# Kernel optimization log

Measured on AMD Instinct MI355X. Metric: run time of the kernel, lower is better.

The kernel has to match this reference:

```python
import jax, jax.numpy as jnp
import numpy as np

D_MODEL, D_STATE, EXPAND, D_CONV, HEADDIM = 1024, 128, 2, 4, 64
D_INNER = EXPAND * D_MODEL                      # 2048
NHEADS = D_INNER // HEADDIM                     # 32
NGROUPS = 1
CONV_DIM = D_INNER + 2 * NGROUPS * D_STATE      # 2304
D_IN_PROJ = 2 * D_INNER + 2 * NGROUPS * D_STATE + NHEADS  # 4384
BATCH, SEQ = 2, 4096
EPS = 1e-5


def setup_inputs() -> dict:
    key = jax.random.key(0)
    ks = jax.random.split(key, 6)
    sn = lambda k, shape, sc: jax.random.normal(k, shape, jnp.float32) * sc
    # dt_bias such that softplus(dt_bias) spans [1e-3, 0.1] (mamba2 init)
    dt = jnp.linspace(1e-3, 0.1, NHEADS)
    return {
        "x": sn(ks[0], (BATCH, SEQ, D_MODEL), 1.0),
        "ln_w": jnp.ones((D_MODEL,), jnp.float32),
        "ln_b": jnp.zeros((D_MODEL,), jnp.float32),
        "in_proj_w": sn(ks[1], (D_IN_PROJ, D_MODEL), D_MODEL ** -0.5),
        "conv_w": sn(ks[2], (CONV_DIM, D_CONV), D_CONV ** -0.5),
        "conv_b": jnp.zeros((CONV_DIM,), jnp.float32),
        "dt_bias": jnp.log(jnp.expm1(dt)).astype(jnp.float32),
        "A_log": jnp.log(jnp.arange(1, NHEADS + 1, dtype=jnp.float32)),
        "D": jnp.ones((NHEADS,), jnp.float32),
        "norm_w": jnp.ones((D_INNER,), jnp.float32),
        "out_proj_w": sn(ks[3], (D_MODEL, D_INNER), D_INNER ** -0.5),
    }


def _mamba2(u, in_proj_w, conv_w, conv_b, dt_bias, A_log, Dp, norm_w, out_proj_w):
    b, l, _ = u.shape
    zxbcdt = u @ in_proj_w.T                              # [b,l,4384]
    z, xBC, dt = jnp.split(zxbcdt, [D_INNER, D_INNER + CONV_DIM], axis=-1)
    # causal depthwise conv1d over channels, then SiLU
    xBC = jnp.transpose(xBC, (0, 2, 1))                   # [b,conv_dim,l]
    xBC = jax.lax.conv_general_dilated(
        xBC, conv_w[:, None, :], window_strides=(1,),
        padding=[(D_CONV - 1, 0)], feature_group_count=CONV_DIM,
        dimension_numbers=("NCH", "OIH", "NCH"))
    xBC = jax.nn.silu(jnp.transpose(xBC, (0, 2, 1)) + conv_b)
    x, Bm, Cm = jnp.split(xBC, [D_INNER, D_INNER + NGROUPS * D_STATE], axis=-1)
    dt = jax.nn.softplus(dt + dt_bias)                    # [b,l,h]
    A = -jnp.exp(A_log)                                   # [h]
    xh = x.reshape(b, l, NHEADS, HEADDIM)
    # time-major for the selective scan
    dt_t, x_t = jnp.moveaxis(dt, 1, 0), jnp.moveaxis(xh, 1, 0)
    B_t, C_t = jnp.moveaxis(Bm, 1, 0), jnp.moveaxis(Cm, 1, 0)

    def step(h, inputs):
        dtk, xk, Bk, Ck = inputs                          # [b,h],[b,h,p],[b,n],[b,n]
        decay = jnp.exp(dtk * A)                          # [b,h]
        h = h * decay[:, :, None, None] + (dtk[:, :, None, None] * xk[..., None]) * Bk[:, None, None, :]
        y = jnp.einsum("bhpn,bn->bhp", h, Ck)
        return h, y

    h0 = jnp.zeros((b, NHEADS, HEADDIM, D_STATE), u.dtype)
    _, ys = jax.lax.scan(step, h0, (dt_t, x_t, B_t, C_t))  # ys: [l,b,h,p]
    y = jnp.moveaxis(ys, 0, 1) + Dp[None, None, :, None] * xh
    y = y.reshape(b, l, D_INNER)
    # gated RMSNorm: rmsnorm(y * silu(z)) * norm_w
    y = y * jax.nn.silu(z)
    y = y * jax.lax.rsqrt(jnp.mean(y * y, axis=-1, keepdims=True) + EPS) * norm_w
    return y @ out_proj_w.T


def reference(x, ln_w, ln_b, in_proj_w, conv_w, conv_b, dt_bias, A_log, D, norm_w, out_proj_w):
    mu = jnp.mean(x, -1, keepdims=True)
    var = jnp.mean((x - mu) ** 2, -1, keepdims=True)
    xn = (x - mu) * jax.lax.rsqrt(var + EPS) * ln_w + ln_b
    # dropout is identity at inference
    return x + _mamba2(xn, in_proj_w, conv_w, conv_b, dt_bias, A_log, D, norm_w, out_proj_w)
```

## Files before the change

kernel.cpp:

```cpp
#include <hip/hip_runtime.h>
#include <cstdint>

#define D_MODEL 1024
#define D_INNER 2048
#define NHEADS 32
#define HEADDIM 64
#define D_STATE 128
#define CONV_DIM 2304
#define D_IN_PROJ 4384
#define SEQ 4096
#define NROWS 8192
#define NPROJ_PAD 4480
#define TCH 128
#define NCHUNK 32
#define CR 8

typedef float f32x4 __attribute__((ext_vector_type(4)));
typedef __bf16 bf16x8 __attribute__((ext_vector_type(8)));
typedef unsigned short u16;

__device__ __forceinline__ u16 f2bf(float f) {
  uint32_t u = __builtin_bit_cast(uint32_t, f);
  u += 0x7FFFu + ((u >> 16) & 1u);
  return (u16)(u >> 16);
}
__device__ __forceinline__ float bf2f(u16 h) {
  return __builtin_bit_cast(float, (uint32_t)h << 16);
}
__device__ __forceinline__ float dexp(float a) { return expf(fminf(0.f, a)); }
__device__ __forceinline__ int sw(int v) { return (((v & 7) ^ ((v >> 3) & 7)) << 3); }

typedef __attribute__((address_space(1))) const void gv_t;
typedef __attribute__((address_space(3))) void lv_t;
__device__ __forceinline__ void gload_lds16(const void* g, void* l) {
  __builtin_amdgcn_global_load_lds((gv_t*)g, (lv_t*)l, 16, 0, 0);
}

__global__ __launch_bounds__(256) void cvt_pad(const float* __restrict__ s,
                                               u16* __restrict__ d, int n_src, int n_dst) {
  int i = (blockIdx.x * 256 + threadIdx.x) * 4;
  int stride = gridDim.x * 256 * 4;
  for (; i < n_dst; i += stride) {
    ushort4 o;
    if (i < n_src) {
      float4 v = *(const float4*)&s[i];
      o.x = f2bf(v.x); o.y = f2bf(v.y); o.z = f2bf(v.z); o.w = f2bf(v.w);
    } else {
      o.x = o.y = o.z = o.w = 0;
    }
    *(ushort4*)&d[i] = o;
  }
}

__global__ __launch_bounds__(256) void ln_kernel(const float* __restrict__ x,
                                                 const float* __restrict__ w,
                                                 const float* __restrict__ b,
                                                 u16* __restrict__ out) {
  int row = blockIdx.x, tid = threadIdx.x;
  const float4 v = *(const float4*)&x[(long)row * D_MODEL + tid * 4];
  float s1 = v.x + v.y + v.z + v.w;
  float s2 = v.x * v.x + v.y * v.y + v.z * v.z + v.w * v.w;
#pragma unroll
  for (int m = 32; m >= 1; m >>= 1) {
    s1 += __shfl_xor(s1, m);
    s2 += __shfl_xor(s2, m);
  }
  __shared__ float p1[4], p2[4];
  if ((tid & 63) == 0) { p1[tid >> 6] = s1; p2[tid >> 6] = s2; }
  __syncthreads();
  s1 = p1[0] + p1[1] + p1[2] + p1[3];
  s2 = p2[0] + p2[1] + p2[2] + p2[3];
  float mean = s1 * (1.f / D_MODEL);
  float var = s2 * (1.f / D_MODEL) - mean * mean;
  float rstd = rsqrtf(var + 1e-5f);
  const float4 wv = *(const float4*)&w[tid * 4];
  const float4 bv = *(const float4*)&b[tid * 4];
  ushort4 o;
  o.x = f2bf((v.x - mean) * rstd * wv.x + bv.x);
  o.y = f2bf((v.y - mean) * rstd * wv.y + bv.y);
  o.z = f2bf((v.z - mean) * rstd * wv.z + bv.z);
  o.w = f2bf((v.w - mean) * rstd * wv.w + bv.w);
  *(ushort4*)&out[(long)row * D_MODEL + tid * 4] = o;
}

template <int MODE>
__global__ __launch_bounds__(256, 4) void gemm_bt(const u16* __restrict__ A,
                                                  const u16* __restrict__ B, int K,
                                                  u16* __restrict__ zb,
                                                  u16* __restrict__ xb,
                                                  float* __restrict__ dtb,
                                                  float* __restrict__ C,
                                                  const float* __restrict__ resid) {
  __shared__ __align__(16) u16 As[128 * 64];
  __shared__ __align__(16) u16 Bs[128 * 64];
  const int tid = threadIdx.x;
  int m0, n0;
  if (MODE == 0) {
    const int k = (blockIdx.x & 7) * 280 + (blockIdx.x >> 3);
    const int st = k / 40, inner = k % 40;
    m0 = ((st & 7) * 8 + (inner & 7)) * 128;
    n0 = ((st >> 3) * 5 + (inner >> 3)) * 128;
  } else {
    const int wg = (blockIdx.x & 7) * 64 + (blockIdx.x >> 3);
    m0 = (wg & 63) * 128;
    n0 = (wg >> 6) * 128;
  }
  const int w = tid >> 6, l = tid & 63;
  const int wm = w >> 1, wn = w & 1;

  f32x4 acc[4][4] = {};

  for (int k0 = 0; k0 < K; k0 += 64) {
#pragma unroll
    for (int i = 0; i < 4; ++i) {
      int idx = i * 256 + tid;
      int row = idx >> 3, slot = idx & 7;
      int ks = slot ^ (row & 7);
      const u16* ga = A + (long)(m0 + row) * K + k0 + ks * 8;
      gload_lds16(ga, (char*)As + idx * 16);
      const u16* gb = B + (long)(n0 + row) * K + k0 + ks * 8;
      gload_lds16(gb, (char*)Bs + idx * 16);
    }
    __syncthreads();
    bf16x8 af[2][4], bfr[2][4];
#pragma unroll
    for (int kk = 0; kk < 2; ++kk)
#pragma unroll
      for (int f = 0; f < 4; ++f) {
        int rowa = wm * 64 + f * 16 + (l & 15);
        int ca = ((kk << 2) | (l >> 4)) ^ (rowa & 7);
        af[kk][f] = *(const bf16x8*)((const char*)As + rowa * 128 + ca * 16);
        int rowb = wn * 64 + f * 16 + (l & 15);
        int cb2 = ((kk << 2) | (l >> 4)) ^ (rowb & 7);
        bfr[kk][f] = *(const bf16x8*)((const char*)Bs + rowb * 128 + cb2 * 16);
      }
#pragma unroll
    for (int kk = 0; kk < 2; ++kk)
#pragma unroll
      for (int mf = 0; mf < 4; ++mf)
#pragma unroll
        for (int nf = 0; nf < 4; ++nf)
          acc[mf][nf] = __builtin_amdgcn_mfma_f32_16x16x32_bf16(
              af[kk][mf], bfr[kk][nf], acc[mf][nf], 0, 0, 0);
    __syncthreads();
  }
#pragma unroll
  for (int mf = 0; mf < 4; ++mf)
#pragma unroll
    for (int nf = 0; nf < 4; ++nf) {
      int col = n0 + wn * 64 + nf * 16 + (l & 15);
#pragma unroll
      for (int r = 0; r < 4; ++r) {
        int rowm = m0 + wm * 64 + mf * 16 + (l >> 4) * 4 + r;
        float v = acc[mf][nf][r];
        if (MODE == 0) {
          if (col < D_INNER)
            zb[(long)rowm * D_INNER + col] = f2bf(v);
          else if (col < D_INNER + CONV_DIM)
            xb[(long)rowm * CONV_DIM + (col - D_INNER)] = f2bf(v);
          else if (col < D_IN_PROJ)
            dtb[(long)rowm * NHEADS + (col - D_INNER - CONV_DIM)] = v;
        } else {
          long off = (long)rowm * D_MODEL + col;
          C[off] = v + resid[off];
        }
      }
    }
}

__global__ __launch_bounds__(256) void conv_silu_kernel(const u16* __restrict__ xr,
                                                        const float* __restrict__ cw,
                                                        const float* __restrict__ cb,
                                                        u16* __restrict__ xp,
                                                        u16* __restrict__ bc) {
  const int c = blockIdx.x * 256 + threadIdx.x;
  const int row0 = blockIdx.y * CR;
  const int t0 = row0 & (SEQ - 1);
  const float4 wv = *(const float4*)&cw[c * 4];
  const float bias = cb[c];
  float xwin[CR + 3];
#pragma unroll
  for (int k = 0; k < CR + 3; ++k) {
    int t = t0 - 3 + k;
    xwin[k] = (t >= 0) ? bf2f(xr[(long)(row0 - 3 + k) * CONV_DIM + c]) : 0.f;
  }
#pragma unroll
  for (int j = 0; j < CR; ++j) {
    float a = bias + xwin[j] * wv.x + xwin[j + 1] * wv.y + xwin[j + 2] * wv.z +
              xwin[j + 3] * wv.w;
    a = a / (1.f + expf(-a));
    int row = row0 + j;
    if (c < D_INNER)
      xp[(long)row * D_INNER + c] = f2bf(a);
    else
      bc[(long)row * (2 * D_STATE) + (c - D_INNER)] = f2bf(a);
  }
}

__global__ __launch_bounds__(256, 3) void ssd_state_kernel(
    const u16* __restrict__ xp, const u16* __restrict__ bcb,
    const float* __restrict__ dtf, const float* __restrict__ dt_bias,
    const float* __restrict__ A_log, u16* __restrict__ S,
    float* __restrict__ cdk) {
  const int hh = blockIdx.x, cc = blockIdx.y, bb = blockIdx.z;
  const int tid = threadIdx.x, w = tid >> 6, l = tid & 63;
  __shared__ __align__(16) u16 BT[128 * 128];
  __shared__ __align__(16) u16 WXT[64 * 128];
  __shared__ float ws[128];
  const long rowbase = (long)bb * SEQ + cc * TCH;
  const float Ah = -expf(A_log[hh]);
  const float dbias = dt_bias[hh];

#pragma unroll
  for (int i = 0; i < 8; ++i) {
    int slot = i * 256 + tid, t = slot >> 4, nb = slot & 15;
    bf16x8 v = *(const bf16x8*)&bcb[(rowbase + t) * 256 + nb * 8];
    const u16* e = (const u16*)&v;
#pragma unroll
    for (int j = 0; j < 8; ++j) {
      int n = nb * 8 + j;
      BT[n * 128 + (t ^ sw(n))] = e[j];
    }
  }
  if (w == 0) {
    float r0 = dtf[(rowbase + l) * NHEADS + hh] + dbias;
    float r1 = dtf[(rowbase + 64 + l) * NHEADS + hh] + dbias;
    float d0 = r0 > 20.f ? r0 : log1pf(expf(r0));
    float d1 = r1 > 20.f ? r1 : log1pf(expf(r1));
    float a0 = d0 * Ah, a1 = d1 * Ah;
#pragma unroll
    for (int d = 1; d < 64; d <<= 1) { float u = __shfl_up(a0, d); if (l >= d) a0 += u; }
#pragma unroll
    for (int d = 1; d < 64; d <<= 1) { float u = __shfl_up(a1, d); if (l >= d) a1 += u; }
    float t0 = __shfl(a0, 63);
    float tot = __shfl(a1, 63) + t0;
    ws[l] = dexp(tot - a0) * d0;
    ws[64 + l] = dexp(tot - (a1 + t0)) * d1;
    if (l == 0) cdk[(bb * 32 + hh) * NCHUNK + cc] = dexp(tot);
  }
  __syncthreads();
#pragma unroll
  for (int i = 0; i < 4; ++i) {
    int slot = i * 256 + tid, t = slot >> 3, pb = slot & 7;
    bf16x8 v = *(const bf16x8*)&xp[(rowbase + t) * D_INNER + hh * 64 + pb * 8];
    float wt = ws[t];
    const u16* e = (const u16*)&v;
#pragma unroll
    for (int j = 0; j < 8; ++j) {
      int p = pb * 8 + j;
      WXT[p * 128 + (t ^ sw(p))] = f2bf(bf2f(e[j]) * wt);
    }
  }
  __syncthreads();

  f32x4 acc[8] = {};
  const int p = w * 16 + (l & 15);
  const int swp = sw(p);
#pragma unroll
  for (int kc = 0; kc < 4; ++kc) {
    int tsl = kc * 32 + (l >> 4) * 8;
    bf16x8 af = *(const bf16x8*)&WXT[p * 128 + (tsl ^ swp)];
#pragma unroll
    for (int nt = 0; nt < 8; ++nt) {
      int n = nt * 16 + (l & 15);
      bf16x8 bfv = *(const bf16x8*)&BT[n * 128 + (tsl ^ sw(n))];
      acc[nt] = __builtin_amdgcn_mfma_f32_16x16x32_bf16(af, bfv, acc[nt], 0, 0, 0);
    }
  }
  u16* Sb = S + ((long)(bb * 32 + hh) * NCHUNK + cc) * 8192;
#pragma unroll
  for (int nt = 0; nt < 8; ++nt)
#pragma unroll
    for (int r = 0; r < 4; ++r) {
      int prow = w * 16 + (l >> 4) * 4 + r;
      Sb[prow * 128 + nt * 16 + (l & 15)] = f2bf(acc[nt][r]);
    }
}

__global__ __launch_bounds__(256) void ssd_combine(u16* __restrict__ SH,
                                                   const float* __restrict__ cdk) {
  const int hh = blockIdx.y, bb = blockIdx.z;
  const int pp = blockIdx.x * 16 + (threadIdx.x >> 4);
  const int nn = (threadIdx.x & 15) * 8;
  const int bh = bb * 32 + hh;
  u16* base = SH + (long)bh * NCHUNK * 8192 + pp * 128 + nn;
  const float* ck = cdk + bh * NCHUNK;
  float h[8] = {};
  for (int c = 0; c < NCHUNK; ++c) {
    bf16x8 sv = *(bf16x8*)(base + (long)c * 8192);
    const u16* se = (const u16*)&sv;
    u16 o[8];
#pragma unroll
    for (int j = 0; j < 8; ++j) o[j] = f2bf(h[j]);
    *(bf16x8*)(base + (long)c * 8192) = *(bf16x8*)o;
    float d = ck[c];
#pragma unroll
    for (int j = 0; j < 8; ++j) h[j] = fmaf(h[j], d, bf2f(se[j]));
  }
}

__global__ __launch_bounds__(256, 2) void ssd_y_kernel(
    const u16* __restrict__ xp, const u16* __restrict__ bcb,
    const float* __restrict__ dtf, const float* __restrict__ dt_bias,
    const float* __restrict__ A_log, const float* __restrict__ Dp,
    const u16* __restrict__ H, u16* __restrict__ y) {
  const int hh = blockIdx.x, cc = blockIdx.y, bb = blockIdx.z;
  const int tid = threadIdx.x, w = tid >> 6, l = tid & 63;
  __shared__ __align__(16) u16 Cs[128 * 128];
  __shared__ __align__(16) u16 XT[64 * 128];
  __shared__ __align__(16) u16 Bp[32 * 128];
  __shared__ __align__(16) u16 Ms[128 * 40];
  __shared__ float sig[128], dts[128], esg[128];
  const long rowbase = (long)bb * SEQ + cc * TCH;
  const float Ah = -expf(A_log[hh]);
  const float Dh = Dp[hh];
  const float dbias = dt_bias[hh];

#pragma unroll
  for (int i = 0; i < 8; ++i) {
    int idx = i * 256 + tid, t = idx >> 4, sl = idx & 15;
    gload_lds16(bcb + (rowbase + t) * 256 + 128 + ((sl ^ (t & 15)) * 8),
                (char*)Cs + idx * 16);
  }
  if (w == 0) {
    float r0 = dtf[(rowbase + l) * NHEADS + hh] + dbias;
    float r1 = dtf[(rowbase + 64 + l) * NHEADS + hh] + dbias;
    float d0 = r0 > 20.f ? r0 : log1pf(expf(r0));
    float d1 = r1 > 20.f ? r1 : log1pf(expf(r1));
    float a0 = d0 * Ah, a1 = d1 * Ah;
#pragma unroll
    for (int d = 1; d < 64; d <<= 1) { float u = __shfl_up(a0, d); if (l >= d) a0 += u; }
#pragma unroll
    for (int d = 1; d < 64; d <<= 1) { float u = __shfl_up(a1, d); if (l >= d) a1 += u; }
    float t0 = __shfl(a0, 63);
    sig[l] = a0; sig[64 + l] = a1 + t0;
    dts[l] = d0; dts[64 + l] = d1;
    esg[l] = dexp(a0); esg[64 + l] = dexp(a1 + t0);
  }
#pragma unroll
  for (int i = 0; i < 4; ++i) {
    int slot = i * 256 + tid, t = slot >> 3, pb = slot & 7;
    bf16x8 v = *(const bf16x8*)&xp[(rowbase + t) * D_INNER + hh * 64 + pb * 8];
    const u16* e = (const u16*)&v;
#pragma unroll
    for (int j = 0; j < 8; ++j) {
      int p = pb * 8 + j;
      XT[p * 128 + (t ^ sw(p))] = e[j];
    }
  }
  __syncthreads();

  bf16x8 cfr[2][4];
#pragma unroll
  for (int tt = 0; tt < 2; ++tt) {
    int t = (w * 2 + tt) * 16 + (l & 15);
#pragma unroll
    for (int kc = 0; kc < 4; ++kc) {
      int sl = (kc * 4 + (l >> 4)) ^ (t & 15);
      cfr[tt][kc] = *(const bf16x8*)&Cs[t * 128 + sl * 8];
    }
  }
  f32x4 y1[2][4] = {};

  for (int sp = 0; sp < 4; ++sp) {
    __syncthreads();
#pragma unroll
    for (int i = 0; i < 2; ++i) {
      int idx = i * 256 + tid, sr = idx >> 4, sl = idx & 15;
      gload_lds16(bcb + (rowbase + sp * 32 + sr) * 256 + ((sl ^ (sr & 15)) * 8),
                  (char*)Bp + idx * 16);
    }
    __syncthreads();
    f32x4 g[2][2] = {};
#pragma unroll
    for (int st = 0; st < 2; ++st)
#pragma unroll
      for (int kc = 0; kc < 4; ++kc) {
        int s = st * 16 + (l & 15);
        int sl = (kc * 4 + (l >> 4)) ^ (s & 15);
        bf16x8 bfv = *(const bf16x8*)&Bp[s * 128 + sl * 8];
        g[0][st] = __builtin_amdgcn_mfma_f32_16x16x32_bf16(cfr[0][kc], bfv, g[0][st], 0, 0, 0);
        g[1][st] = __builtin_amdgcn_mfma_f32_16x16x32_bf16(cfr[1][kc], bfv, g[1][st], 0, 0, 0);
      }
#pragma unroll
    for (int tt = 0; tt < 2; ++tt)
#pragma unroll
      for (int st = 0; st < 2; ++st)
#pragma unroll
        for (int r = 0; r < 4; ++r) {
          int t = (w * 2 + tt) * 16 + (l >> 4) * 4 + r;
          int s = sp * 32 + st * 16 + (l & 15);
          float m = 0.f;
          if (s <= t) m = g[tt][st][r] * dexp(sig[t] - sig[s]) * dts[s];
          Ms[t * 40 + st * 16 + (l & 15)] = f2bf(m);
        }
    __syncthreads();
#pragma unroll
    for (int tt = 0; tt < 2; ++tt) {
      int t = (w * 2 + tt) * 16 + (l & 15);
      bf16x8 mf = *(const bf16x8*)&Ms[t * 40 + (l >> 4) * 8];
#pragma unroll
      for (int pt = 0; pt < 4; ++pt) {
        int p = pt * 16 + (l & 15);
        int ssl = sp * 32 + (l >> 4) * 8;
        bf16x8 xf = *(const bf16x8*)&XT[p * 128 + (ssl ^ sw(p))];
        y1[tt][pt] = __builtin_amdgcn_mfma_f32_16x16x32_bf16(mf, xf, y1[tt][pt], 0, 0, 0);
      }
    }
  }
  f32x4 y2[2][4] = {};
  const u16* Hb = H + ((long)(bb * 32 + hh) * NCHUNK + cc) * 8192;
#pragma unroll
  for (int pt = 0; pt < 4; ++pt) {
    int p = pt * 16 + (l & 15);
#pragma unroll
    for (int kc = 0; kc < 4; ++kc) {
      bf16x8 hf = *(const bf16x8*)&Hb[p * 128 + kc * 32 + (l >> 4) * 8];
      y2[0][pt] = __builtin_amdgcn_mfma_f32_16x16x32_bf16(cfr[0][kc], hf, y2[0][pt], 0, 0, 0);
      y2[1][pt] = __builtin_amdgcn_mfma_f32_16x16x32_bf16(cfr[1][kc], hf, y2[1][pt], 0, 0, 0);
    }
  }
#pragma unroll
  for (int tt = 0; tt < 2; ++tt)
#pragma unroll
    for (int pt = 0; pt < 4; ++pt)
#pragma unroll
      for (int r = 0; r < 4; ++r) {
        int t = (w * 2 + tt) * 16 + (l >> 4) * 4 + r;
        int p = pt * 16 + (l & 15);
        float xv = bf2f(XT[p * 128 + (t ^ sw(p))]);
        float yv = y1[tt][pt][r] + esg[t] * y2[tt][pt][r] + Dh * xv;
        y[(rowbase + t) * (long)D_INNER + hh * 64 + p] = f2bf(yv);
      }
}

__global__ __launch_bounds__(256) void grms_kernel(const u16* __restrict__ yb,
                                                   u16* __restrict__ zb,
                                                   const float* __restrict__ nw) {
  int row = blockIdx.x, tid = threadIdx.x;
  const u16* yp = yb + (long)row * D_INNER + tid * 8;
  u16* zp = zb + (long)row * D_INNER + tid * 8;
  ushort4 yv0 = *(const ushort4*)yp, yv1 = *(const ushort4*)(yp + 4);
  ushort4 zv0 = *(const ushort4*)zp, zv1 = *(const ushort4*)(zp + 4);
  u16 ya[8] = {yv0.x, yv0.y, yv0.z, yv0.w, yv1.x, yv1.y, yv1.z, yv1.w};
  u16 za[8] = {zv0.x, zv0.y, zv0.z, zv0.w, zv1.x, zv1.y, zv1.z, zv1.w};
  float g[8];
  float s2 = 0.f;
#pragma unroll
  for (int j = 0; j < 8; ++j) {
    float z = bf2f(za[j]);
    float gg = bf2f(ya[j]) * (z / (1.f + expf(-z)));
    g[j] = gg;
    s2 += gg * gg;
  }
#pragma unroll
  for (int m = 32; m >= 1; m >>= 1) s2 += __shfl_xor(s2, m);
  __shared__ float p2[4];
  if ((tid & 63) == 0) p2[tid >> 6] = s2;
  __syncthreads();
  s2 = p2[0] + p2[1] + p2[2] + p2[3];
  float r = rsqrtf(s2 * (1.f / D_INNER) + 1e-5f);
  const float4 w0 = *(const float4*)&nw[tid * 8];
  const float4 w1 = *(const float4*)&nw[tid * 8 + 4];
  const float* wp = (const float*)&w0;
  const float* wq = (const float*)&w1;
  ushort4 o0, o1;
  o0.x = f2bf(g[0] * r * wp[0]); o0.y = f2bf(g[1] * r * wp[1]);
  o0.z = f2bf(g[2] * r * wp[2]); o0.w = f2bf(g[3] * r * wp[3]);
  o1.x = f2bf(g[4] * r * wq[0]); o1.y = f2bf(g[5] * r * wq[1]);
  o1.z = f2bf(g[6] * r * wq[2]); o1.w = f2bf(g[7] * r * wq[3]);
  *(ushort4*)zp = o0;
  *(ushort4*)(zp + 4) = o1;
}

extern "C" void kernel_launch(void* const* d_in, const int* in_sizes, int n_in,
                              void* d_out, int out_size, void* d_ws, size_t ws_size,
                              hipStream_t stream) {
  const float* x = (const float*)d_in[0];
  const float* ln_w = (const float*)d_in[1];
  const float* ln_b = (const float*)d_in[2];
  const float* in_proj_w = (const float*)d_in[3];
  const float* conv_w = (const float*)d_in[4];
  const float* conv_b = (const float*)d_in[5];
  const float* dt_bias = (const float*)d_in[6];
  const float* A_log = (const float*)d_in[7];
  const float* Dvec = (const float*)d_in[8];
  const float* norm_w = (const float*)d_in[9];
  const float* out_proj_w = (const float*)d_in[10];
  float* out = (float*)d_out;

  char* ws = (char*)d_ws;
  u16* W2bf = (u16*)(ws + 0);
  u16* zbf = (u16*)(ws + 4194304);
  u16* xpart = (u16*)(ws + 37748736);
  u16* bcbf = (u16*)(ws + 71303168);
  float* dtf = (float*)(ws + 75497472);
  float* cdk = (float*)(ws + 76546048);
  u16* W1bf = (u16*)(ws + 76554240);
  u16* xbcraw = (u16*)(ws + 85729280);
  u16* SH = (u16*)(ws + 76554240);
  u16* xnbf = (u16*)d_out;
  u16* ybf = (u16*)d_out;

  cvt_pad<<<512, 256, 0, stream>>>(in_proj_w, W1bf, D_IN_PROJ * D_MODEL,
                                   NPROJ_PAD * D_MODEL);
  cvt_pad<<<512, 256, 0, stream>>>(out_proj_w, W2bf, D_MODEL * D_INNER,
                                   D_MODEL * D_INNER);
  ln_kernel<<<NROWS, 256, 0, stream>>>(x, ln_w, ln_b, xnbf);
  gemm_bt<0><<<35 * 64, 256, 0, stream>>>(xnbf, W1bf, D_MODEL, zbf, xbcraw, dtf,
                                          nullptr, nullptr);
  conv_silu_kernel<<<dim3(9, NROWS / CR), 256, 0, stream>>>(xbcraw, conv_w, conv_b,
                                                            xpart, bcbf);
  ssd_state_kernel<<<dim3(32, NCHUNK, 2), 256, 0, stream>>>(xpart, bcbf, dtf, dt_bias,
                                                            A_log, SH, cdk);
  ssd_combine<<<dim3(4, 32, 2), 256, 0, stream>>>(SH, cdk);
  ssd_y_kernel<<<dim3(32, NCHUNK, 2), 256, 0, stream>>>(xpart, bcbf, dtf, dt_bias,
                                                        A_log, Dvec, SH, ybf);
  grms_kernel<<<NROWS, 256, 0, stream>>>(ybf, zbf, norm_w);
  gemm_bt<1><<<8 * 64, 256, 0, stream>>>(zbf, W2bf, D_INNER, nullptr, nullptr,
                                         nullptr, out, x);
}
```

Before: 296.0 us.

## Fuse gated RMSNorm into SSD output and fold scaling into out-proj GEMM

The SiLU(z) gating now happens in the ssd_y epilogue, which writes the gated values straight into the z buffer and emits per-head partial sums of squares. A tiny r_reduce kernel turns these into per-row rsqrt factors. norm_w is folded into the bf16 out_proj weights during conversion, and the row factor is applied in the out-proj GEMM epilogue. This removes the grms_kernel and the y round trip through memory. In exchange the ssd_y epilogue does scattered 2-byte loads and stores of z, and rounding now happens before normalization.

```diff
diff --git a/kernel.cpp b/kernel.cpp
--- a/kernel.cpp
+++ b/kernel.cpp
@@ -48,6 +48,23 @@
     } else {
       o.x = o.y = o.z = o.w = 0;
     }
+    *(ushort4*)&d[i] = o;
+  }
+}
+
+__global__ __launch_bounds__(256) void cvt_w2s(const float* __restrict__ s,
+                                               const float* __restrict__ nw,
+                                               u16* __restrict__ d, int n) {
+  int i = (blockIdx.x * 256 + threadIdx.x) * 4;
+  int stride = gridDim.x * 256 * 4;
+  for (; i < n; i += stride) {
+    float4 v = *(const float4*)&s[i];
+    int c = i & (D_INNER - 1);
+    ushort4 o;
+    o.x = f2bf(v.x * nw[c]);
+    o.y = f2bf(v.y * nw[c + 1]);
+    o.z = f2bf(v.z * nw[c + 2]);
+    o.w = f2bf(v.w * nw[c + 3]);
     *(ushort4*)&d[i] = o;
   }
 }
@@ -90,7 +107,8 @@
                                                   u16* __restrict__ xb,
                                                   float* __restrict__ dtb,
                                                   float* __restrict__ C,
-                                                  const float* __restrict__ resid) {
+                                                  const float* __restrict__ resid,
+                                                  const float* __restrict__ rvec) {
   __shared__ __align__(16) u16 As[128 * 64];
   __shared__ __align__(16) u16 Bs[128 * 64];
   const int tid = threadIdx.x;
@@ -162,7 +180,7 @@
             dtb[(long)rowm * NHEADS + (col - D_INNER - CONV_DIM)] = v;
         } else {
           long off = (long)rowm * D_MODEL + col;
-          C[off] = v + resid[off];
+          C[off] = v * rvec[rowm] + resid[off];
         }
       }
     }
@@ -303,7 +321,8 @@
     const u16* __restrict__ xp, const u16* __restrict__ bcb,
     const float* __restrict__ dtf, const float* __restrict__ dt_bias,
     const float* __restrict__ A_log, const float* __restrict__ Dp,
-    const u16* __restrict__ H, u16* __restrict__ y) {
+    const u16* __restrict__ H, u16* __restrict__ zb,
+    float* __restrict__ psum) {
   const int hh = blockIdx.x, cc = blockIdx.y, bb = blockIdx.z;
   const int tid = threadIdx.x, w = tid >> 6, l = tid & 63;
   __shared__ __align__(16) u16 Cs[128 * 128];
@@ -420,6 +439,7 @@
       y2[1][pt] = __builtin_amdgcn_mfma_f32_16x16x32_bf16(cfr[1][kc], hf, y2[1][pt], 0, 0, 0);
     }
   }
+  float s2[2][4] = {};
 #pragma unroll
   for (int tt = 0; tt < 2; ++tt)
 #pragma unroll
@@ -430,47 +450,39 @@
         int p = pt * 16 + (l & 15);
         float xv = bf2f(XT[p * 128 + (t ^ sw(p))]);
         float yv = y1[tt][pt][r] + esg[t] * y2[tt][pt][r] + Dh * xv;
-        y[(rowbase + t) * (long)D_INNER + hh * 64 + p] = f2bf(yv);
+        long off = (rowbase + t) * (long)D_INNER + hh * 64 + p;
+        float zv = bf2f(zb[off]);
+        float gg = yv * (zv / (1.f + expf(-zv)));
+        zb[off] = f2bf(gg);
+        s2[tt][r] += gg * gg;
       }
-}
-
-__global__ __launch_bounds__(256) void grms_kernel(const u16* __restrict__ yb,
-                                                   u16* __restrict__ zb,
-                                                   const float* __restrict__ nw) {
-  int row = blockIdx.x, tid = threadIdx.x;
-  const u16* yp = yb + (long)row * D_INNER + tid * 8;
-  u16* zp = zb + (long)row * D_INNER + tid * 8;
-  ushort4 yv0 = *(const ushort4*)yp, yv1 = *(const ushort4*)(yp + 4);
-  ushort4 zv0 = *(const ushort4*)zp, zv1 = *(const ushort4*)(zp + 4);
-  u16 ya[8] = {yv0.x, yv0.y, yv0.z, yv0.w, yv1.x, yv1.y, yv1.z, yv1.w};
-  u16 za[8] = {zv0.x, zv0.y, zv0.z, zv0.w, zv1.x, zv1.y, zv1.z, zv1.w};
-  float g[8];
-  float s2 = 0.f;
-#pragma unroll
-  for (int j = 0; j < 8; ++j) {
-    float z = bf2f(za[j]);
-    float gg = bf2f(ya[j]) * (z / (1.f + expf(-z)));
-    g[j] = gg;
-    s2 += gg * gg;
-  }
-#pragma unroll
-  for (int m = 32; m >= 1; m >>= 1) s2 += __shfl_xor(s2, m);
-  __shared__ float p2[4];
-  if ((tid & 63) == 0) p2[tid >> 6] = s2;
-  __syncthreads();
-  s2 = p2[0] + p2[1] + p2[2] + p2[3];
-  float r = rsqrtf(s2 * (1.f / D_INNER) + 1e-5f);
-  const float4 w0 = *(const float4*)&nw[tid * 8];
-  const float4 w1 = *(const float4*)&nw[tid * 8 + 4];
-  const float* wp = (const float*)&w0;
-  const float* wq = (const float*)&w1;
-  ushort4 o0, o1;
-  o0.x = f2bf(g[0] * r * wp[0]); o0.y = f2bf(g[1] * r * wp[1]);
-  o0.z = f2bf(g[2] * r * wp[2]); o0.w = f2bf(g[3] * r * wp[3]);
-  o1.x = f2bf(g[4] * r * wq[0]); o1.y = f2bf(g[5] * r * wq[1]);
-  o1.z = f2bf(g[6] * r * wq[2]); o1.w = f2bf(g[7] * r * wq[3]);
-  *(ushort4*)zp = o0;
-  *(ushort4*)(zp + 4) = o1;
+#pragma unroll
+  for (int tt = 0; tt < 2; ++tt)
+#pragma unroll
+    for (int r = 0; r < 4; ++r) {
+      float v = s2[tt][r];
+      v += __shfl_xor(v, 1);
+      v += __shfl_xor(v, 2);
+      v += __shfl_xor(v, 4);
+      v += __shfl_xor(v, 8);
+      if ((l & 15) == 0) {
+        int t = (w * 2 + tt) * 16 + (l >> 4) * 4 + r;
+        psum[(rowbase + t) * NHEADS + hh] = v;
+      }
+    }
+}
+
+__global__ __launch_bounds__(256) void r_reduce(const float* __restrict__ psum,
+                                                float* __restrict__ rvec) {
+  int row = blockIdx.x * 256 + threadIdx.x;
+  const float4* p = (const float4*)&psum[(long)row * NHEADS];
+  float s = 0.f;
+#pragma unroll
+  for (int i = 0; i < 8; ++i) {
+    float4 v = p[i];
+    s += v.x + v.y + v.z + v.w;
+  }
+  rvec[row] = rsqrtf(s * (1.f / D_INNER) + 1e-5f);
 }
 
 extern "C" void kernel_launch(void* const* d_in, const int* in_sizes, int n_in,
@@ -499,24 +511,24 @@
   u16* W1bf = (u16*)(ws + 76554240);
   u16* xbcraw = (u16*)(ws + 85729280);
   u16* SH = (u16*)(ws + 76554240);
+  float* psum = (float*)(ws + 110108672);
+  float* rvec = (float*)(ws + 111157248);
   u16* xnbf = (u16*)d_out;
-  u16* ybf = (u16*)d_out;
 
   cvt_pad<<<512, 256, 0, stream>>>(in_proj_w, W1bf, D_IN_PROJ * D_MODEL,
                                    NPROJ_PAD * D_MODEL);
-  cvt_pad<<<512, 256, 0, stream>>>(out_proj_w, W2bf, D_MODEL * D_INNER,
-                                   D_MODEL * D_INNER);
+  cvt_w2s<<<512, 256, 0, stream>>>(out_proj_w, norm_w, W2bf, D_MODEL * D_INNER);
   ln_kernel<<<NROWS, 256, 0, stream>>>(x, ln_w, ln_b, xnbf);
   gemm_bt<0><<<35 * 64, 256, 0, stream>>>(xnbf, W1bf, D_MODEL, zbf, xbcraw, dtf,
-                                          nullptr, nullptr);
+                                          nullptr, nullptr, nullptr);
   conv_silu_kernel<<<dim3(9, NROWS / CR), 256, 0, stream>>>(xbcraw, conv_w, conv_b,
                                                             xpart, bcbf);
   ssd_state_kernel<<<dim3(32, NCHUNK, 2), 256, 0, stream>>>(xpart, bcbf, dtf, dt_bias,
                                                             A_log, SH, cdk);
   ssd_combine<<<dim3(4, 32, 2), 256, 0, stream>>>(SH, cdk);
   ssd_y_kernel<<<dim3(32, NCHUNK, 2), 256, 0, stream>>>(xpart, bcbf, dtf, dt_bias,
-                                                        A_log, Dvec, SH, ybf);
-  grms_kernel<<<NROWS, 256, 0, stream>>>(ybf, zbf, norm_w);
+                                                        A_log, Dvec, SH, zbf, psum);
+  r_reduce<<<32, 256, 0, stream>>>(psum, rvec);
   gemm_bt<1><<<8 * 64, 256, 0, stream>>>(zbf, W2bf, D_INNER, nullptr, nullptr,
-                                         nullptr, out, x);
-}
+                                         nullptr, out, x, rvec);
+}
```

Result: no change. 295.6 us (-0.1%).
